# Kernel tuning notes

Measured on AMD Instinct MI355X. Metric: run time of the kernel, lower is better.

Reference implementation:

```python
import jax, jax.numpy as jnp
import numpy as np

EPS_BN = 1e-4


def gcn_conv(x, W, b, src, dst):
    """PyG GCNConv with added self-loops and symmetric normalization."""
    N = x.shape[0]
    h = x @ W  # [N, out]
    # degree over targets, +1 for the implicit self-loop on every node
    deg = jnp.zeros((N,), x.dtype).at[dst].add(1.0) + 1.0
    dinv = jax.lax.rsqrt(deg)  # deg^{-1/2}
    norm = dinv[src] * dinv[dst]  # per-edge coefficient
    msg = h[src] * norm[:, None]  # [E, out] gather (memory-bound)
    out = jax.ops.segment_sum(msg, dst, num_segments=N)
    out = out + h * (dinv * dinv)[:, None]  # self-loop term, norm = 1/deg
    return out + b


def batch_norm(x, gamma, beta):
    # training-mode BN over the node dim, biased variance (matches torch train)
    m = jnp.mean(x, axis=0)
    v = jnp.mean(jnp.square(x - m), axis=0)
    return (x - m) * jax.lax.rsqrt(v + EPS_BN) * gamma + beta


def setup_inputs() -> dict:
    key = jax.random.key(0)
    ks = jax.random.split(key, 8)
    N, E, D = 100000, 1600000, 64
    L = 2
    x = jax.random.normal(ks[0], (N, D), jnp.float32)
    edge_index = jax.random.randint(ks[1], (2, E), 0, N, jnp.int32)
    batch = jnp.sort(jax.random.randint(ks[2], (N,), 0, 128, jnp.int32))
    s = 1.0 / np.sqrt(D)
    return {
        "x": x,
        "edge_index": edge_index,
        "batch": batch,
        "enc_W": jax.random.normal(ks[3], (L, D, D), jnp.float32) * s,
        "enc_b": jnp.zeros((L, D), jnp.float32),
        "enc_gamma": jnp.ones((L, D), jnp.float32),
        "enc_beta": jnp.zeros((L, D), jnp.float32),
        "attr_W": jax.random.normal(ks[4], (L, D, D), jnp.float32) * s,
        "attr_b": jnp.zeros((L, D), jnp.float32),
        "attr_gamma": jnp.ones((L, D), jnp.float32),
        "attr_beta": jnp.zeros((L, D), jnp.float32),
        "str_W": jax.random.normal(ks[5], (L, D, D), jnp.float32) * s,
        "str_b": jnp.zeros((L, D), jnp.float32),
        "str_gamma": jnp.ones((L, D), jnp.float32),
        "str_beta": jnp.zeros((L, D), jnp.float32),
    }


def reference(x, edge_index, batch, enc_W, enc_b, enc_gamma, enc_beta,
              attr_W, attr_b, attr_gamma, attr_beta,
              str_W, str_b, str_gamma, str_beta):
    src, dst = edge_index[0], edge_index[1]
    L = enc_W.shape[0]

    # ---- Encoder: GCN -> sigmoid -> (dropout id) -> BN ----
    h = x
    for i in range(L):
        h = gcn_conv(h, enc_W[i], enc_b[i], src, dst)
        h = jax.nn.sigmoid(h)
        h = batch_norm(h, enc_gamma[i], enc_beta[i])
    x_enc = h
    # x_pool = global_mean_pool(x_enc, batch) is computed but discarded upstream

    # ---- Attribute decoder: GCN -> (dropout) -> sigmoid (except last) -> BN ----
    h = x_enc
    for i in range(L):
        h = gcn_conv(h, attr_W[i], attr_b[i], src, dst)
        if i != L - 1:
            h = jax.nn.sigmoid(h)
        h = batch_norm(h, attr_gamma[i], attr_beta[i])
    x_att = h

    # ---- Structure decoder ----
    h = x_enc
    for i in range(L):
        h = gcn_conv(h, str_W[i], str_b[i], src, dst)
        if i != L - 1:
            h = jax.nn.sigmoid(h)
        else:
            h = jax.nn.sigmoid(h * 0.5)
        h = batch_norm(h, str_gamma[i], str_beta[i])
    x_str = h

    return (x_str, x_att, x_enc)
```

## Files before the change

kernel.cpp:

```cpp
#include <hip/hip_runtime.h>

#define D 64
#define BCH 4096

typedef __attribute__((ext_vector_type(8))) _Float16 f16x8;
typedef __attribute__((ext_vector_type(4))) float f32x4;

__device__ __forceinline__ float sigmoidf_(float x) {
    return 1.0f / (1.0f + __expf(-x));
}
__device__ __forceinline__ float h2f(ushort u) {
    _Float16 h;
    __builtin_memcpy(&h, &u, 2);
    return (float)h;
}
__device__ __forceinline__ ushort f2h(float f) {
    _Float16 h = (_Float16)f;
    ushort u;
    __builtin_memcpy(&u, &h, 2);
    return u;
}
__device__ __forceinline__ float2 up2(uint v) {
    float2 r;
    r.x = h2f((ushort)(v & 0xffffu));
    r.y = h2f((ushort)(v >> 16));
    return r;
}


__global__ __launch_bounds__(256) void bin_edges(const int* __restrict__ src,
                                                 const int* __restrict__ dst,
                                                 int* __restrict__ bcur,
                                                 int* __restrict__ binsrc,
                                                 int* __restrict__ bindst,
                                                 int CAP, int E) {
    __shared__ int lsrc[BCH], ldst[BCH];
    __shared__ int hist[128], base[128];
    int t = threadIdx.x;
    int e0 = blockIdx.x * BCH;
    if (t < 128) hist[t] = 0;
    __syncthreads();
    for (int k = t; k < BCH; k += 256) {
        int e = e0 + k;
        int d_ = -1, s_ = 0;
        if (e < E) {
            s_ = src[e];
            d_ = dst[e];
            atomicAdd(&hist[d_ >> 10], 1);
        }
        lsrc[k] = s_;
        ldst[k] = d_;
    }
    __syncthreads();
    if (t < 128) {
        int c = hist[t];
        base[t] = (c > 0) ? atomicAdd(&bcur[t], c) : 0;
        hist[t] = 0;
    }
    __syncthreads();
    for (int k = t; k < BCH; k += 256) {
        int d_ = ldst[k];
        if (d_ >= 0) {
            int b = d_ >> 10;
            int p = base[b] + atomicAdd(&hist[b], 1);
            binsrc[(size_t)b * CAP + p] = lsrc[k];
            bindst[(size_t)b * CAP + p] = d_;
        }
    }
}

__global__ __launch_bounds__(128) void scan_nb(const int* __restrict__ bcur,
                                               int* __restrict__ boff,
                                               int* __restrict__ csr,
                                               int NB, int N, int E) {
    __shared__ int tmp[128];
    int t = threadIdx.x;
    int v = (t < NB) ? bcur[t] : 0;
    tmp[t] = v;
    __syncthreads();
    for (int o = 1; o < 128; o <<= 1) {
        int x = (t >= o) ? tmp[t - o] : 0;
        __syncthreads();
        tmp[t] += x;
        __syncthreads();
    }
    if (t < NB) boff[t] = tmp[t] - v;
    if (t == 0) csr[N] = E;
}

__global__ __launch_bounds__(256) void build_csr(const int* __restrict__ binsrc,
                                                 const int* __restrict__ bindst,
                                                 const int* __restrict__ bcur,
                                                 const int* __restrict__ boff,
                                                 int* __restrict__ csr,
                                                 int* __restrict__ sorted,
                                                 float* __restrict__ dinv,
                                                 float* __restrict__ rdinv,
                                                 int CAP, int N) {
    __shared__ int hist[1024];
    __shared__ int part[256];
    int t = threadIdx.x;
    int b = blockIdx.x;
    int nb0 = b << 10;
    int cnt = bcur[b];
    int e0 = boff[b];
    const int* bs = binsrc + (size_t)b * CAP;
    const int* bd = bindst + (size_t)b * CAP;
    for (int k = t; k < 1024; k += 256) hist[k] = 0;
    __syncthreads();
    for (int k = t; k < cnt; k += 256) atomicAdd(&hist[bd[k] - nb0], 1);
    __syncthreads();
    int v0 = hist[4 * t], v1 = hist[4 * t + 1], v2 = hist[4 * t + 2], v3 = hist[4 * t + 3];
    part[t] = v0 + v1 + v2 + v3;
    __syncthreads();
    for (int o = 1; o < 256; o <<= 1) {
        int x = (t >= o) ? part[t - o] : 0;
        __syncthreads();
        part[t] += x;
        __syncthreads();
    }
    int run = (t > 0) ? part[t - 1] : 0;
    int pre[4];
    pre[0] = run;
    pre[1] = run + v0;
    pre[2] = run + v0 + v1;
    pre[3] = run + v0 + v1 + v2;
    int deg[4] = {v0, v1, v2, v3};
    __syncthreads();
    hist[4 * t + 0] = e0 + pre[0];
    hist[4 * t + 1] = e0 + pre[1];
    hist[4 * t + 2] = e0 + pre[2];
    hist[4 * t + 3] = e0 + pre[3];
#pragma unroll
    for (int j = 0; j < 4; j++) {
        int node = nb0 + 4 * t + j;
        if (node < N) {
            csr[node] = e0 + pre[j];
            float c = (float)deg[j] + 1.0f;
            dinv[node] = rsqrtf(c);
            rdinv[node] = sqrtf(c);
        }
    }
    __syncthreads();
    for (int k = t; k < cnt; k += 256) {
        int d_ = bd[k];
        int p = atomicAdd(&hist[d_ - nb0], 1);
        sorted[p] = bs[k];
    }
}


__global__ __launch_bounds__(256) void prep_xd(const float* __restrict__ x,
                                               const float* __restrict__ dinv,
                                               ushort* __restrict__ actd, int N16) {
    int p = blockIdx.x * 256 + threadIdx.x;
    if (p >= N16) return;
    int n = p >> 4;
    float d = dinv[n];
    float4 v = reinterpret_cast<const float4*>(x)[p];
    ushort4 o;
    o.x = f2h(v.x * d);
    o.y = f2h(v.y * d);
    o.z = f2h(v.z * d);
    o.w = f2h(v.w * d);
    reinterpret_cast<ushort4*>(actd)[p] = o;
}

__global__ __launch_bounds__(256) void wprep(const float* __restrict__ W,
                                             ushort* __restrict__ wfrag) {
    int idx = blockIdx.x * 256 + threadIdx.x;
    if (idx >= 4096) return;
    int i = idx & 7;
    int lane = (idx >> 3) & 63;
    int hc = idx >> 9;
    int h = hc >> 2, c = hc & 3;
    int k = h * 32 + (lane >> 4) * 8 + i;
    int j = c * 16 + (lane & 15);
    wfrag[idx] = f2h(W[k * 64 + j]);
}

__global__ __launch_bounds__(256) void layer_prep(const float* __restrict__ ssum,
                                                  const float* __restrict__ sssq,
                                                  const float* __restrict__ gamma,
                                                  const float* __restrict__ beta,
                                                  const float* __restrict__ W,
                                                  float* __restrict__ A,
                                                  float* __restrict__ C,
                                                  float* __restrict__ u,
                                                  ushort* __restrict__ wfrag,
                                                  float invN) {
    __shared__ float As[64], Cs[64];
    int t = threadIdx.x;
    if (t < 64) {
        float m = ssum[t] * invN;
        float var = sssq[t] * invN - m * m;
        float rs = rsqrtf(var + 1e-4f);
        float a = rs * gamma[t];
        As[t] = a;
        A[t] = a;
        float c = fmaf(-m, a, beta[t]);
        Cs[t] = c;
        C[t] = c;
    }
    __syncthreads();
    if (t < 64) {
        float s = 0.f;
        for (int k = 0; k < 64; k++) s = fmaf(Cs[k], W[k * 64 + t], s);
        u[t] = s;
    }
    for (int idx = t; idx < 4096; idx += 256) {
        int i = idx & 7;
        int lane = (idx >> 3) & 63;
        int hc = idx >> 9;
        int h = hc >> 2, c = hc & 3;
        int k = h * 32 + (lane >> 4) * 8 + i;
        int j = c * 16 + (lane & 15);
        wfrag[idx] = f2h(W[k * 64 + j] * As[k]);
    }
}

__global__ __launch_bounds__(64) void finalize_aff(const float* __restrict__ ssum,
                                                   const float* __restrict__ sssq,
                                                   const float* __restrict__ gamma,
                                                   const float* __restrict__ beta,
                                                   float* __restrict__ A,
                                                   float* __restrict__ C, float invN) {
    int c = threadIdx.x;
    float m = ssum[c] * invN;
    float var = sssq[c] * invN - m * m;
    float rs = rsqrtf(var + 1e-4f);
    float a = rs * gamma[c];
    A[c] = a;
    C[c] = fmaf(-m, a, beta[c]);
}


__global__ __launch_bounds__(256) void agg_g(const ushort* __restrict__ actd,
                                             const int* __restrict__ ptr,
                                             const int* __restrict__ srcs,
                                             const float* __restrict__ dinv,
                                             const float* __restrict__ rdinv,
                                             ushort* __restrict__ zh,
                                             float* __restrict__ ssum,
                                             float* __restrict__ sssq,
                                             float* __restrict__ qout, int N, int E) {
    __shared__ float red[2][4][64];
    int lane = threadIdx.x & 63;
    int wv = threadIdx.x >> 6;
    int Em1 = E - 1;
    const bool do_stats = (ssum != nullptr);
    const bool do_q = (qout != nullptr);
    float ps = 0.f, pq = 0.f;
    for (int n = blockIdx.x * 4 + wv; n < N; n += gridDim.x * 4) {
        int s = ptr[n], e = ptr[n + 1];
        float self = h2f(actd[((size_t)n << 6) + lane]);
        float acc = self;
        float dn = dinv[n];
        if (do_stats) {
            float a = self * rdinv[n];
            ps += a;
            pq += a * a;
        }
        float qa = 0.f;
        int i = s;
        int idx8 = srcs[min(i + (lane & 7), Em1)];
        while (i + 8 <= e) {
            int ni = i + 8;
            int nidx = srcs[min(ni + (lane & 7), Em1)];
#pragma unroll
            for (int j = 0; j < 8; j++) {
                int u = __builtin_amdgcn_readlane(idx8, j);
                float f = h2f(actd[((size_t)u << 6) + lane]);
                acc += f;
                if (do_q) qa += dinv[u];
            }
            idx8 = nidx;
            i = ni;
        }
        if (i < e) {
#pragma unroll
            for (int j = 0; j < 8; j++) {
                int u = __builtin_amdgcn_readlane(idx8, j);
                float f = h2f(actd[((size_t)u << 6) + lane]);
                float w = (i + j < e) ? 1.0f : 0.0f;
                acc = fmaf(w, f, acc);
                if (do_q) qa = fmaf(w, dinv[u], qa);
            }
        }
        if (do_q && lane == 0) qout[n] = dn * (dn + qa);
        zh[((size_t)n << 6) + lane] = f2h(acc * dn);
    }
    if (do_stats) {
        red[0][wv][lane] = ps;
        red[1][wv][lane] = pq;
        __syncthreads();
        if (wv == 0) {
            float t0 = red[0][0][lane] + red[0][1][lane] + red[0][2][lane] + red[0][3][lane];
            float t1 = red[1][0][lane] + red[1][1][lane] + red[1][2][lane] + red[1][3][lane];
            atomicAdd(&ssum[lane], t0);
            atomicAdd(&sssq[lane], t1);
        }
    }
}

__global__ __launch_bounds__(256) void agg_dual(const ushort* __restrict__ ab,
                                                const int* __restrict__ ptr,
                                                const int* __restrict__ srcs,
                                                const float* __restrict__ dinv,
                                                const float* __restrict__ rdinv,
                                                ushort* __restrict__ zab,
                                                float* __restrict__ ssA,
                                                float* __restrict__ sqA,
                                                float* __restrict__ ssS,
                                                float* __restrict__ sqS,
                                                int N, int E) {
    __shared__ float red[2][4][128];
    int lane = threadIdx.x & 63;
    int wv = threadIdx.x >> 6;
    int Em1 = E - 1;
    float2 ps = make_float2(0.f, 0.f), pq = make_float2(0.f, 0.f);
    for (int n = blockIdx.x * 4 + wv; n < N; n += gridDim.x * 4) {
        int s = ptr[n], e = ptr[n + 1];
        uint su = *reinterpret_cast<const uint*>(ab + ((size_t)n << 7) + (lane << 1));
        float2 acc = up2(su);
        {
            float r = rdinv[n];
            float ax = acc.x * r, ay = acc.y * r;
            ps.x += ax; ps.y += ay;
            pq.x += ax * ax; pq.y += ay * ay;
        }
        int i = s;
        int idx8 = srcs[min(i + (lane & 7), Em1)];
        while (i + 8 <= e) {
            int ni = i + 8;
            int nidx = srcs[min(ni + (lane & 7), Em1)];
#pragma unroll
            for (int j = 0; j < 8; j++) {
                int u = __builtin_amdgcn_readlane(idx8, j);
                uint v = *reinterpret_cast<const uint*>(ab + ((size_t)u << 7) + (lane << 1));
                float2 f = up2(v);
                acc.x += f.x;
                acc.y += f.y;
            }
            idx8 = nidx;
            i = ni;
        }
        if (i < e) {
#pragma unroll
            for (int j = 0; j < 8; j++) {
                int u = __builtin_amdgcn_readlane(idx8, j);
                uint v = *reinterpret_cast<const uint*>(ab + ((size_t)u << 7) + (lane << 1));
                float w = (i + j < e) ? 1.0f : 0.0f;
                float2 f = up2(v);
                acc.x = fmaf(w, f.x, acc.x);
                acc.y = fmaf(w, f.y, acc.y);
            }
        }
        float dn = dinv[n];
        uint pk = (uint)f2h(acc.x * dn) | ((uint)f2h(acc.y * dn) << 16);
        *reinterpret_cast<uint*>(zab + ((size_t)n << 7) + (lane << 1)) = pk;
    }
    red[0][wv][2 * lane + 0] = ps.x;
    red[0][wv][2 * lane + 1] = ps.y;
    red[1][wv][2 * lane + 0] = pq.x;
    red[1][wv][2 * lane + 1] = pq.y;
    __syncthreads();
    if (wv == 0) {
#pragma unroll
        for (int m0 = 0; m0 < 2; m0++) {
            int m = lane + m0 * 64;
            float t0 = red[0][0][m] + red[0][1][m] + red[0][2][m] + red[0][3][m];
            float t1 = red[1][0][m] + red[1][1][m] + red[1][2][m] + red[1][3][m];
            if (m < 64) {
                atomicAdd(&ssA[m], t0);
                atomicAdd(&sqA[m], t1);
            } else {
                atomicAdd(&ssS[m - 64], t0);
                atomicAdd(&sqS[m - 64], t1);
            }
        }
    }
}

template <int MODE, bool HAS_AFF, int OM>
__global__ __launch_bounds__(256) void gemm_mfma(const ushort* __restrict__ zh, int is,
                                                 const ushort* __restrict__ wfrag,
                                                 const float* __restrict__ bias,
                                                 const float* __restrict__ u,
                                                 const float* __restrict__ q,
                                                 const float* __restrict__ dinv,
                                                 ushort* __restrict__ outh, int os,
                                                 float* __restrict__ outf,
                                                 float* __restrict__ s0,
                                                 float* __restrict__ s1, int N) {
    int tid = threadIdx.x;
    int lane = tid & 63;
    int wv = tid >> 6;
    int l15 = lane & 15;
    int lg = lane >> 4;
    int tb = blockIdx.x * 64;

    const ushort* zrow = zh + (size_t)(tb + wv * 16 + l15) * is + (lg << 3);
    f16x8 a0 = *reinterpret_cast<const f16x8*>(zrow);
    f16x8 a1 = *reinterpret_cast<const f16x8*>(zrow + 32);

    const f16x8* wf = reinterpret_cast<const f16x8*>(wfrag) + lane;

    f32x4 acc[4];
#pragma unroll
    for (int c = 0; c < 4; c++) {
        f32x4 t = {0.f, 0.f, 0.f, 0.f};
        t = __builtin_amdgcn_mfma_f32_16x16x32_f16(a0, wf[(0 * 4 + c) * 64], t, 0, 0, 0);
        t = __builtin_amdgcn_mfma_f32_16x16x32_f16(a1, wf[(1 * 4 + c) * 64], t, 0, 0, 0);
        acc[c] = t;
    }

    int rowbase = tb + wv * 16 + lg * 4;
    float qv[4], dv[4];
    bool vld[4];
#pragma unroll
    for (int r = 0; r < 4; r++) {
        int row = rowbase + r;
        vld[r] = row < N;
        qv[r] = (HAS_AFF && vld[r]) ? q[row] : 0.f;
        dv[r] = (OM == 0 && vld[r]) ? dinv[row] : 0.f;
    }
    float sa[4], sq[4];
#pragma unroll
    for (int c = 0; c < 4; c++) { sa[c] = 0.f; sq[c] = 0.f; }

#pragma unroll
    for (int c = 0; c < 4; c++) {
        int col = c * 16 + l15;
        float bcol = bias[col];
        float ucol = HAS_AFF ? u[col] : 0.f;
        float Acol = (OM == 2) ? s0[col] : 0.f;
        float Ccol = (OM == 2) ? s1[col] : 0.f;
#pragma unroll
        for (int r = 0; r < 4; r++) {
            if (!vld[r]) continue;
            float o = acc[c][r] + bcol;
            if (HAS_AFF) o = fmaf(qv[r], ucol, o);
            float a = (MODE == 0) ? sigmoidf_(o)
// ... 66 lines not shown
    for (int c = 0; c < 4; c++) {
        f32x4 t = {0.f, 0.f, 0.f, 0.f};
        t = __builtin_amdgcn_mfma_f32_16x16x32_f16(a0, wa[(0 * 4 + c) * 64], t, 0, 0, 0);
        t = __builtin_amdgcn_mfma_f32_16x16x32_f16(a1, wa[(1 * 4 + c) * 64], t, 0, 0, 0);
        accA[c] = t;
        f32x4 t2 = {0.f, 0.f, 0.f, 0.f};
        t2 = __builtin_amdgcn_mfma_f32_16x16x32_f16(a0, wsp[(0 * 4 + c) * 64], t2, 0, 0, 0);
        t2 = __builtin_amdgcn_mfma_f32_16x16x32_f16(a1, wsp[(1 * 4 + c) * 64], t2, 0, 0, 0);
        accS[c] = t2;
    }

    int rowbase = tb + wv * 16 + lg * 4;
    float qv[4], dv[4];
    bool vld[4];
#pragma unroll
    for (int r = 0; r < 4; r++) {
        int row = rowbase + r;
        vld[r] = row < N;
        qv[r] = vld[r] ? q[row] : 0.f;
        dv[r] = vld[r] ? dinv[row] : 0.f;
    }
#pragma unroll
    for (int c = 0; c < 4; c++) {
        int col = c * 16 + l15;
        float bcA = bA[col], ucA = uA[col];
        float bcS = bS[col], ucS = uS[col];
#pragma unroll
        for (int r = 0; r < 4; r++) {
            if (!vld[r]) continue;
            int row = rowbase + r;
            float oA = fmaf(qv[r], ucA, accA[c][r] + bcA);
            float oS = fmaf(qv[r], ucS, accS[c][r] + bcS);
            float aA = sigmoidf_(oA);
            float aS = sigmoidf_(oS);
            outAB[((size_t)row << 7) + col] = f2h(aA * dv[r]);
            outAB[((size_t)row << 7) + 64 + col] = f2h(aS * dv[r]);
        }
    }
}

__global__ __launch_bounds__(256) void bn_apply_h(const ushort* __restrict__ actd,
                                                  const float* __restrict__ rdinv,
                                                  const float* __restrict__ A,
                                                  const float* __restrict__ C,
                                                  float* __restrict__ out, int N16) {
    int p = blockIdx.x * 256 + threadIdx.x;
    if (p >= N16) return;
    int n = p >> 4;
    int cb = (p & 15) * 4;
    float r = rdinv[n];
    ushort4 v = reinterpret_cast<const ushort4*>(actd)[p];
    float4 o;
    o.x = fmaf(h2f(v.x) * r, A[cb + 0], C[cb + 0]);
    o.y = fmaf(h2f(v.y) * r, A[cb + 1], C[cb + 1]);
    o.z = fmaf(h2f(v.z) * r, A[cb + 2], C[cb + 2]);
    o.w = fmaf(h2f(v.w) * r, A[cb + 3], C[cb + 3]);
    reinterpret_cast<float4*>(out)[p] = o;
}


extern "C" void kernel_launch(void* const* d_in, const int* in_sizes, int n_in,
                              void* d_out, int out_size, void* d_ws, size_t ws_size,
                              hipStream_t stream) {
    const int N = in_sizes[0] / D;
    const int E = in_sizes[1] / 2;

    const float* x = (const float*)d_in[0];
    const int* ei = (const int*)d_in[1];
    const int* src_in = ei;
    const int* dst_in = ei + E;
    const float* encW = (const float*)d_in[3];
    const float* encb = (const float*)d_in[4];
    const float* encg = (const float*)d_in[5];
    const float* encbe = (const float*)d_in[6];
    const float* attW = (const float*)d_in[7];
    const float* attb = (const float*)d_in[8];
    const float* attg = (const float*)d_in[9];
    const float* attbe = (const float*)d_in[10];
    const float* strW = (const float*)d_in[11];
    const float* strb = (const float*)d_in[12];
    const float* strg = (const float*)d_in[13];
    const float* strbe = (const float*)d_in[14];

    const int NB = (N + 1023) >> 10;
    int CAP = (E + NB - 1) / NB;
    CAP = CAP + CAP / 8 + 256;
    CAP = (CAP + 255) & ~255;

    char* ws = (char*)d_ws;
    size_t off = 0;
    auto alloc = [&](size_t bytes) -> char* {
        char* p = ws + off;
        off += (bytes + 255) & ~(size_t)255;
        return p;
    };
    int* csr = (int*)alloc((size_t)(N + 1) * 4);
    int* bcur = (int*)alloc(128 * 4);
    int* boff = (int*)alloc(128 * 4);
    float* dinv = (float*)alloc((size_t)N * 4);
    float* rdinv = (float*)alloc((size_t)N * 4);
    float* q = (float*)alloc((size_t)N * 4);
    float* stats = (float*)alloc(6 * 128 * 4);
    float* aff = (float*)alloc(6 * 128 * 4);
    float* ubuf = (float*)alloc(6 * 64 * 4);
    ushort* wf = (ushort*)alloc(6 * 4096 * 2);
    int* sorted = (int*)alloc((size_t)E * 4);
    ushort* zh = (ushort*)alloc((size_t)(N + 64) * 64 * 2);
    size_t binbytes = 2 * (size_t)NB * CAP * 4;
    size_t zabbytes = (size_t)(N + 64) * 128 * 2;
    char* region = alloc(binbytes > zabbytes ? binbytes : zabbytes);
    int* binsrc = (int*)region;
    int* bindst = binsrc + (size_t)NB * CAP;
    ushort* zab = (ushort*)region;
    ushort* hA = (ushort*)alloc((size_t)N * 64 * 2);
    ushort* hB = (ushort*)alloc((size_t)N * 64 * 2);
    ushort* hAB = (ushort*)alloc((size_t)(N + 64) * 128 * 2);

    float* out_str = (float*)d_out;
    float* out_att = out_str + (size_t)N * D;
    float* out_enc = out_att + (size_t)N * D;

    hipMemsetAsync(bcur, 0, 128 * 4, stream);
    hipMemsetAsync(stats, 0, 6 * 128 * 4, stream);

    int N16 = N * 16;
    int g16 = (N16 + 255) / 256;
    int gT = (N + 63) / 64;
    float invN = 1.0f / (float)N;

    float* A0 = aff + 0 * 128; float* C0 = A0 + 64;
    float* A1 = aff + 1 * 128; float* C1 = A1 + 64;
    float* A2 = aff + 2 * 128; float* C2 = A2 + 64;
    float* A3 = aff + 3 * 128; float* C3 = A3 + 64;
    float* A4 = aff + 4 * 128; float* C4 = A4 + 64;
    float* A5 = aff + 5 * 128; float* C5 = A5 + 64;
    ushort* wf0 = wf + 0 * 4096;
    ushort* wf1 = wf + 1 * 4096;
    ushort* wf2 = wf + 2 * 4096;
    ushort* wf3 = wf + 3 * 4096;
    ushort* wf4 = wf + 4 * 4096;
    ushort* wf5 = wf + 5 * 4096;

    bin_edges<<<(E + BCH - 1) / BCH, 256, 0, stream>>>(src_in, dst_in, bcur,
                                                       binsrc, bindst, CAP, E);
    scan_nb<<<1, 128, 0, stream>>>(bcur, boff, csr, NB, N, E);
    build_csr<<<NB, 256, 0, stream>>>(binsrc, bindst, bcur, boff, csr, sorted,
                                      dinv, rdinv, CAP, N);

    prep_xd<<<g16, 256, 0, stream>>>(x, dinv, hA, N16);
    wprep<<<16, 256, 0, stream>>>(encW, wf0);
    agg_g<<<2048, 256, 0, stream>>>(hA, csr, sorted, dinv, rdinv, zh,
                                    nullptr, nullptr, q, N, E);
    gemm_mfma<0, false, 0><<<gT, 256, 0, stream>>>(zh, 64, wf0, encb, nullptr,
                                                   q, dinv, hB, 64, nullptr,
                                                   nullptr, nullptr, N);
    agg_g<<<2048, 256, 0, stream>>>(hB, csr, sorted, dinv, rdinv, zh,
                                    stats + 0, stats + 64, nullptr, N, E);
    layer_prep<<<1, 256, 0, stream>>>(stats + 0, stats + 64, encg, encbe,
                                      encW + 4096, A0, C0, ubuf + 0, wf1, invN);
    gemm_mfma<0, true, 0><<<gT, 256, 0, stream>>>(zh, 64, wf1, encb + 64, ubuf + 0,
                                                  q, dinv, hA, 64, nullptr,
                                                  nullptr, nullptr, N);
    agg_g<<<2048, 256, 0, stream>>>(hA, csr, sorted, dinv, rdinv, zh,
                                    stats + 128, stats + 192, nullptr, N, E);
    layer_prep<<<1, 256, 0, stream>>>(stats + 128, stats + 192, encg + 64,
                                      encbe + 64, attW, A1, C1, ubuf + 64, wf2, invN);
    layer_prep<<<1, 256, 0, stream>>>(stats + 128, stats + 192, encg + 64,
                                      encbe + 64, strW, A1, C1, ubuf + 128, wf3, invN);
    bn_apply_h<<<g16, 256, 0, stream>>>(hA, rdinv, A1, C1, out_enc, N16);
    gemm_dual<<<gT, 256, 0, stream>>>(zh, wf2, wf3, attb, strb, ubuf + 64,
                                      ubuf + 128, q, dinv, hAB, N);
    agg_dual<<<2048, 256, 0, stream>>>(hAB, csr, sorted, dinv, rdinv, zab,
                                       stats + 256, stats + 320,
                                       stats + 512, stats + 576, N, E);
    layer_prep<<<1, 256, 0, stream>>>(stats + 256, stats + 320, attg, attbe,
                                      attW + 4096, A2, C2, ubuf + 192, wf4, invN);
    gemm_mfma<1, true, 1><<<gT, 256, 0, stream>>>(zab, 128, wf4, attb + 64,
                                                  ubuf + 192, q, dinv, nullptr, 0,
                                                  nullptr, stats + 384, stats + 448, N);
    finalize_aff<<<1, 64, 0, stream>>>(stats + 384, stats + 448, attg + 64,
                                       attbe + 64, A3, C3, invN);
    gemm_mfma<1, true, 2><<<gT, 256, 0, stream>>>(zab, 128, wf4, attb + 64,
                                                  ubuf + 192, q, dinv, nullptr, 0,
                                                  out_att, A3, C3, N);
    layer_prep<<<1, 256, 0, stream>>>(stats + 512, stats + 576, strg, strbe,
                                      strW + 4096, A4, C4, ubuf + 320, wf5, invN);
    gemm_mfma<2, true, 1><<<gT, 256, 0, stream>>>(zab + 64, 128, wf5, strb + 64,
                                                  ubuf + 320, q, dinv, nullptr, 0,
                                                  nullptr, stats + 640, stats + 704, N);
    finalize_aff<<<1, 64, 0, stream>>>(stats + 640, stats + 704, strg + 64,
                                       strbe + 64, A5, C5, invN);
    gemm_mfma<2, true, 2><<<gT, 256, 0, stream>>>(zab + 64, 128, wf5, strb + 64,
                                                  ubuf + 320, q, dinv, nullptr, 0,
                                                  out_str, A5, C5, N);
}
```

Baseline: 604.9 us.

## Pack edge bins into single word and interleave two nodes per wave in aggregation

Edge binning now packs the source index and the low 10 bits of the destination into one 32-bit word, which halves the global traffic for binned edges and the local memory used by the binning kernel. Both aggregation kernels now have each wave process two nodes from opposite halves of the node range in an interleaved loop. This puts more independent gathers in flight per wave to hide memory latency. The cost is more registers and divergent control flow when the two nodes' degrees differ, and the packing assumes the source index fits in 22 bits.

```diff
diff --git a/kernel.cpp b/kernel.cpp
--- a/kernel.cpp
+++ b/kernel.cpp
@@ -31,10 +31,10 @@
 __global__ __launch_bounds__(256) void bin_edges(const int* __restrict__ src,
                                                  const int* __restrict__ dst,
                                                  int* __restrict__ bcur,
-                                                 int* __restrict__ binsrc,
-                                                 int* __restrict__ bindst,
+                                                 uint* __restrict__ bins,
                                                  int CAP, int E) {
-    __shared__ int lsrc[BCH], ldst[BCH];
+    __shared__ uint lp[BCH];
+    __shared__ unsigned char lb[BCH];
     __shared__ int hist[128], base[128];
     int t = threadIdx.x;
     int e0 = blockIdx.x * BCH;
@@ -42,14 +42,17 @@
     __syncthreads();
     for (int k = t; k < BCH; k += 256) {
         int e = e0 + k;
-        int d_ = -1, s_ = 0;
+        uint p = 0xFFFFFFFFu;
+        int b = 0;
         if (e < E) {
-            s_ = src[e];
-            d_ = dst[e];
-            atomicAdd(&hist[d_ >> 10], 1);
-        }
-        lsrc[k] = s_;
-        ldst[k] = d_;
+            int s_ = src[e];
+            int d_ = dst[e];
+            b = d_ >> 10;
+            atomicAdd(&hist[b], 1);
+            p = ((uint)s_ << 10) | (uint)(d_ & 1023);
+        }
+        lp[k] = p;
+        lb[k] = (unsigned char)b;
     }
     __syncthreads();
     if (t < 128) {
@@ -59,12 +62,11 @@
     }
     __syncthreads();
     for (int k = t; k < BCH; k += 256) {
-        int d_ = ldst[k];
-        if (d_ >= 0) {
-            int b = d_ >> 10;
-            int p = base[b] + atomicAdd(&hist[b], 1);
-            binsrc[(size_t)b * CAP + p] = lsrc[k];
-            bindst[(size_t)b * CAP + p] = d_;
+        uint p = lp[k];
+        if (p != 0xFFFFFFFFu) {
+            int b = lb[k];
+            int pos = base[b] + atomicAdd(&hist[b], 1);
+            bins[(size_t)b * CAP + pos] = p;
         }
     }
 }
@@ -88,8 +90,7 @@
     if (t == 0) csr[N] = E;
 }
 
-__global__ __launch_bounds__(256) void build_csr(const int* __restrict__ binsrc,
-                                                 const int* __restrict__ bindst,
+__global__ __launch_bounds__(256) void build_csr(const uint* __restrict__ bins,
                                                  const int* __restrict__ bcur,
                                                  const int* __restrict__ boff,
                                                  int* __restrict__ csr,
@@ -104,11 +105,10 @@
     int nb0 = b << 10;
     int cnt = bcur[b];
     int e0 = boff[b];
-    const int* bs = binsrc + (size_t)b * CAP;
-    const int* bd = bindst + (size_t)b * CAP;
+    const uint* bp = bins + (size_t)b * CAP;
     for (int k = t; k < 1024; k += 256) hist[k] = 0;
     __syncthreads();
-    for (int k = t; k < cnt; k += 256) atomicAdd(&hist[bd[k] - nb0], 1);
+    for (int k = t; k < cnt; k += 256) atomicAdd(&hist[bp[k] & 1023u], 1);
     __syncthreads();
     int v0 = hist[4 * t], v1 = hist[4 * t + 1], v2 = hist[4 * t + 2], v3 = hist[4 * t + 3];
     part[t] = v0 + v1 + v2 + v3;
@@ -143,9 +143,9 @@
     }
     __syncthreads();
     for (int k = t; k < cnt; k += 256) {
-        int d_ = bd[k];
-        int p = atomicAdd(&hist[d_ - nb0], 1);
-        sorted[p] = bs[k];
+        uint p = bp[k];
+        int pos = atomicAdd(&hist[p & 1023u], 1);
+        sorted[pos] = (int)(p >> 10);
     }
 }
 
@@ -247,48 +247,106 @@
     __shared__ float red[2][4][64];
     int lane = threadIdx.x & 63;
     int wv = threadIdx.x >> 6;
+    int l7 = lane & 7;
     int Em1 = E - 1;
     const bool do_stats = (ssum != nullptr);
     const bool do_q = (qout != nullptr);
     float ps = 0.f, pq = 0.f;
-    for (int n = blockIdx.x * 4 + wv; n < N; n += gridDim.x * 4) {
-        int s = ptr[n], e = ptr[n + 1];
-        float self = h2f(actd[((size_t)n << 6) + lane]);
-        float acc = self;
-        float dn = dinv[n];
+    int Nh = (N + 1) >> 1;
+    for (int n0 = blockIdx.x * 4 + wv; n0 < Nh; n0 += gridDim.x * 4) {
+        int nA = n0;
+        int nB = n0 + Nh;
+        bool hasB = nB < N;
+        int sA = ptr[nA], eA = ptr[nA + 1];
+        int sB = 0, eB = 0;
+        if (hasB) { sB = ptr[nB]; eB = ptr[nB + 1]; }
+        float selfA = h2f(actd[((size_t)nA << 6) + lane]);
+        float accA = selfA;
+        float dnA = dinv[nA];
+        float accB = 0.f, dnB = 0.f;
+        if (hasB) {
+            float selfB = h2f(actd[((size_t)nB << 6) + lane]);
+            accB = selfB;
+            dnB = dinv[nB];
+            if (do_stats) {
+                float rb = rdinv[nB];
+                float b = selfB * rb;
+                ps += b;
+                pq += b * b;
+            }
+        }
         if (do_stats) {
-            float a = self * rdinv[n];
+            float ra = rdinv[nA];
+            float a = selfA * ra;
             ps += a;
             pq += a * a;
         }
-        float qa = 0.f;
-        int i = s;
-        int idx8 = srcs[min(i + (lane & 7), Em1)];
-        while (i + 8 <= e) {
-            int ni = i + 8;
-            int nidx = srcs[min(ni + (lane & 7), Em1)];
+        float qaA = 0.f, qaB = 0.f;
+        int iA = sA, iB = sB;
+        int idxA = srcs[min(iA + l7, Em1)];
+        int idxB = hasB ? srcs[min(iB + l7, Em1)] : 0;
+        while (iA + 8 <= eA || iB + 8 <= eB) {
+            bool gA = iA + 8 <= eA;
+            bool gB = iB + 8 <= eB;
+            ushort ua[8], ub[8];
+            if (gA) {
+#pragma unroll
+                for (int j = 0; j < 8; j++) {
+                    int u = __builtin_amdgcn_readlane(idxA, j);
+                    ua[j] = actd[((size_t)u << 6) + lane];
+                    if (do_q) qaA += dinv[u];
+                }
+            }
+            if (gB) {
+#pragma unroll
+                for (int j = 0; j < 8; j++) {
+                    int u = __builtin_amdgcn_readlane(idxB, j);
+                    ub[j] = actd[((size_t)u << 6) + lane];
+                    if (do_q) qaB += dinv[u];
+                }
+            }
+            int idxA2 = idxA, idxB2 = idxB;
+            if (gA) idxA2 = srcs[min(iA + 8 + l7, Em1)];
+            if (gB) idxB2 = srcs[min(iB + 8 + l7, Em1)];
+            if (gA) {
+                accA += ((h2f(ua[0]) + h2f(ua[1])) + (h2f(ua[2]) + h2f(ua[3]))) +
+                        ((h2f(ua[4]) + h2f(ua[5])) + (h2f(ua[6]) + h2f(ua[7])));
+                iA += 8;
+                idxA = idxA2;
+            }
+            if (gB) {
+                accB += ((h2f(ub[0]) + h2f(ub[1])) + (h2f(ub[2]) + h2f(ub[3]))) +
+                        ((h2f(ub[4]) + h2f(ub[5])) + (h2f(ub[6]) + h2f(ub[7])));
+                iB += 8;
+                idxB = idxB2;
+            }
+        }
+        if (iA < eA) {
 #pragma unroll
             for (int j = 0; j < 8; j++) {
-                int u = __builtin_amdgcn_readlane(idx8, j);
+                int u = __builtin_amdgcn_readlane(idxA, j);
+                float w = (iA + j < eA) ? 1.0f : 0.0f;
                 float f = h2f(actd[((size_t)u << 6) + lane]);
-                acc += f;
-                if (do_q) qa += dinv[u];
-            }
-            idx8 = nidx;
-            i = ni;
-        }
-        if (i < e) {
+                accA = fmaf(w, f, accA);
+                if (do_q) qaA = fmaf(w, dinv[u], qaA);
+            }
+        }
+        if (hasB && iB < eB) {
 #pragma unroll
             for (int j = 0; j < 8; j++) {
-                int u = __builtin_amdgcn_readlane(idx8, j);
+                int u = __builtin_amdgcn_readlane(idxB, j);
+                float w = (iB + j < eB) ? 1.0f : 0.0f;
                 float f = h2f(actd[((size_t)u << 6) + lane]);
-                float w = (i + j < e) ? 1.0f : 0.0f;
-                acc = fmaf(w, f, acc);
-                if (do_q) qa = fmaf(w, dinv[u], qa);
-            }
-        }
-        if (do_q && lane == 0) qout[n] = dn * (dn + qa);
-        zh[((size_t)n << 6) + lane] = f2h(acc * dn);
+                accB = fmaf(w, f, accB);
+                if (do_q) qaB = fmaf(w, dinv[u], qaB);
+            }
+        }
+        if (do_q && lane == 0) {
+            qout[nA] = dnA * (dnA + qaA);
+            if (hasB) qout[nB] = dnB * (dnB + qaB);
+        }
+        zh[((size_t)nA << 6) + lane] = f2h(accA * dnA);
+        if (hasB) zh[((size_t)nB << 6) + lane] = f2h(accB * dnB);
     }
     if (do_stats) {
         red[0][wv][lane] = ps;
@@ -317,48 +375,110 @@
     __shared__ float red[2][4][128];
     int lane = threadIdx.x & 63;
     int wv = threadIdx.x >> 6;
+    int l7 = lane & 7;
     int Em1 = E - 1;
     float2 ps = make_float2(0.f, 0.f), pq = make_float2(0.f, 0.f);
-    for (int n = blockIdx.x * 4 + wv; n < N; n += gridDim.x * 4) {
-        int s = ptr[n], e = ptr[n + 1];
-        uint su = *reinterpret_cast<const uint*>(ab + ((size_t)n << 7) + (lane << 1));
-        float2 acc = up2(su);
+    int Nh = (N + 1) >> 1;
+    for (int n0 = blockIdx.x * 4 + wv; n0 < Nh; n0 += gridDim.x * 4) {
+        int nA = n0;
+        int nB = n0 + Nh;
+        bool hasB = nB < N;
+        int sA = ptr[nA], eA = ptr[nA + 1];
+        int sB = 0, eB = 0;
+        if (hasB) { sB = ptr[nB]; eB = ptr[nB + 1]; }
+        uint suA = *reinterpret_cast<const uint*>(ab + ((size_t)nA << 7) + (lane << 1));
+        float2 accA = up2(suA);
+        float dnA = dinv[nA];
         {
-            float r = rdinv[n];
-            float ax = acc.x * r, ay = acc.y * r;
+            float r = rdinv[nA];
+            float ax = accA.x * r, ay = accA.y * r;
             ps.x += ax; ps.y += ay;
             pq.x += ax * ax; pq.y += ay * ay;
         }
-        int i = s;
-        int idx8 = srcs[min(i + (lane & 7), Em1)];
-        while (i + 8 <= e) {
-            int ni = i + 8;
-            int nidx = srcs[min(ni + (lane & 7), Em1)];
+        float2 accB = make_float2(0.f, 0.f);
+        float dnB = 0.f;
+        if (hasB) {
+            uint suB = *reinterpret_cast<const uint*>(ab + ((size_t)nB << 7) + (lane << 1));
+            accB = up2(suB);
+            dnB = dinv[nB];
+            float r = rdinv[nB];
+            float ax = accB.x * r, ay = accB.y * r;
+            ps.x += ax; ps.y += ay;
+            pq.x += ax * ax; pq.y += ay * ay;
+        }
+        int iA = sA, iB = sB;
+        int idxA = srcs[min(iA + l7, Em1)];
+        int idxB = hasB ? srcs[min(iB + l7, Em1)] : 0;
+        while (iA + 8 <= eA || iB + 8 <= eB) {
+            bool gA = iA + 8 <= eA;
+            bool gB = iB + 8 <= eB;
+            uint va[8], vb[8];
+            if (gA) {
+#pragma unroll
+                for (int j = 0; j < 8; j++) {
+                    int u = __builtin_amdgcn_readlane(idxA, j);
+                    va[j] = *reinterpret_cast<const uint*>(ab + ((size_t)u << 7) + (lane << 1));
+                }
+            }
+            if (gB) {
+#pragma unroll
+                for (int j = 0; j < 8; j++) {
+                    int u = __builtin_amdgcn_readlane(idxB, j);
+                    vb[j] = *reinterpret_cast<const uint*>(ab + ((size_t)u << 7) + (lane << 1));
+                }
+            }
+            int idxA2 = idxA, idxB2 = idxB;
+            if (gA) idxA2 = srcs[min(iA + 8 + l7, Em1)];
+            if (gB) idxB2 = srcs[min(iB + 8 + l7, Em1)];
+            if (gA) {
+#pragma unroll
+                for (int j = 0; j < 8; j++) {
+                    float2 f = up2(va[j]);
+                    accA.x += f.x;
+                    accA.y += f.y;
+                }
+                iA += 8;
+                idxA = idxA2;
+            }
+            if (gB) {
+#pragma unroll
+                for (int j = 0; j < 8; j++) {
+                    float2 f = up2(vb[j]);
+                    accB.x += f.x;
+                    accB.y += f.y;
+                }
+                iB += 8;
+                idxB = idxB2;
+            }
+        }
+        if (iA < eA) {
 #pragma unroll
             for (int j = 0; j < 8; j++) {
-                int u = __builtin_amdgcn_readlane(idx8, j);
+                int u = __builtin_amdgcn_readlane(idxA, j);
                 uint v = *reinterpret_cast<const uint*>(ab + ((size_t)u << 7) + (lane << 1));
+                float w = (iA + j < eA) ? 1.0f : 0.0f;
                 float2 f = up2(v);
-                acc.x += f.x;
-                acc.y += f.y;
-            }
-            idx8 = nidx;
-            i = ni;
-        }
-        if (i < e) {
+                accA.x = fmaf(w, f.x, accA.x);
+                accA.y = fmaf(w, f.y, accA.y);
+            }
+        }
+        if (hasB && iB < eB) {
 #pragma unroll
             for (int j = 0; j < 8; j++) {
-                int u = __builtin_amdgcn_readlane(idx8, j);
+                int u = __builtin_amdgcn_readlane(idxB, j);
                 uint v = *reinterpret_cast<const uint*>(ab + ((size_t)u << 7) + (lane << 1));
-                float w = (i + j < e) ? 1.0f : 0.0f;
+                float w = (iB + j < eB) ? 1.0f : 0.0f;
                 float2 f = up2(v);
-                acc.x = fmaf(w, f.x, acc.x);
-                acc.y = fmaf(w, f.y, acc.y);
-            }
-        }
-        float dn = dinv[n];
-        uint pk = (uint)f2h(acc.x * dn) | ((uint)f2h(acc.y * dn) << 16);
-        *reinterpret_cast<uint*>(zab + ((size_t)n << 7) + (lane << 1)) = pk;
+                accB.x = fmaf(w, f.x, accB.x);
+                accB.y = fmaf(w, f.y, accB.y);
+            }
+        }
+        uint pkA = (uint)f2h(accA.x * dnA) | ((uint)f2h(accA.y * dnA) << 16);
+        *reinterpret_cast<uint*>(zab + ((size_t)nA << 7) + (lane << 1)) = pkA;
+        if (hasB) {
+            uint pkB = (uint)f2h(accB.x * dnB) | ((uint)f2h(accB.y * dnB) << 16);
+            *reinterpret_cast<uint*>(zab + ((size_t)nB << 7) + (lane << 1)) = pkB;
+        }
     }
     red[0][wv][2 * lane + 0] = ps.x;
     red[0][wv][2 * lane + 1] = ps.y;
@@ -615,11 +735,10 @@
     ushort* wf = (ushort*)alloc(6 * 4096 * 2);
     int* sorted = (int*)alloc((size_t)E * 4);
     ushort* zh = (ushort*)alloc((size_t)(N + 64) * 64 * 2);
-    size_t binbytes = 2 * (size_t)NB * CAP * 4;
+    size_t binbytes = (size_t)NB * CAP * 4;
     size_t zabbytes = (size_t)(N + 64) * 128 * 2;
     char* region = alloc(binbytes > zabbytes ? binbytes : zabbytes);
-    int* binsrc = (int*)region;
-    int* bindst = binsrc + (size_t)NB * CAP;
+    uint* bins = (uint*)region;
     ushort* zab = (ushort*)region;
     ushort* hA = (ushort*)alloc((size_t)N * 64 * 2);
     ushort* hB = (ushort*)alloc((size_t)N * 64 * 2);
@@ -651,9 +770,9 @@
     ushort* wf5 = wf + 5 * 4096;
 
     bin_edges<<<(E + BCH - 1) / BCH, 256, 0, stream>>>(src_in, dst_in, bcur,
-                                                       binsrc, bindst, CAP, E);
+                                                       bins, CAP, E);
     scan_nb<<<1, 128, 0, stream>>>(bcur, boff, csr, NB, N, E);
-    build_csr<<<NB, 256, 0, stream>>>(binsrc, bindst, bcur, boff, csr, sorted,
+    build_csr<<<NB, 256, 0, stream>>>(bins, bcur, boff, csr, sorted,
                                       dinv, rdinv, CAP, N);
 
     prep_xd<<<g16, 256, 0, stream>>>(x, dinv, hA, N16);
```

After: 602.8 us. About the same (-0.3%).

## Partition CSR edges by source slab to improve gather locality

Applied to the files above, without the earlier changes.

Edges are now binned by (source slab of 8192 nodes, destination block), producing 16 separate CSR segments per node so that the edges stored in each bin come from a narrow source range. Aggregation kernels walk the 16 segments in order, aiming to keep gathered feature rows within a cache-friendly window. Bins pack src and local dst into one 32-bit word, and degree/dinv moves to a separate kernel summing the 16 segment lengths. This costs 16 CSR pointer reads per node, many short segments with partial 8-edge groups, and a loss of cross-group index prefetch in the gather loop.

```diff
diff --git a/kernel.cpp b/kernel.cpp
--- a/kernel.cpp
+++ b/kernel.cpp
@@ -2,6 +2,8 @@
 
 #define D 64
 #define BCH 4096
+#define NS 16
+#define SSH 13
 
 typedef __attribute__((ext_vector_type(8))) _Float16 f16x8;
 typedef __attribute__((ext_vector_type(4))) float f32x4;
@@ -31,84 +33,102 @@
 __global__ __launch_bounds__(256) void bin_edges(const int* __restrict__ src,
                                                  const int* __restrict__ dst,
                                                  int* __restrict__ bcur,
-                                                 int* __restrict__ binsrc,
-                                                 int* __restrict__ bindst,
-                                                 int CAP, int E) {
-    __shared__ int lsrc[BCH], ldst[BCH];
-    __shared__ int hist[128], base[128];
+                                                 uint* __restrict__ bins,
+                                                 int CAP, int NBd, int NB2, int E) {
+    __shared__ uint lp[BCH];
+    __shared__ ushort lb[BCH];
+    __shared__ int hist[1600], base[1600];
     int t = threadIdx.x;
     int e0 = blockIdx.x * BCH;
-    if (t < 128) hist[t] = 0;
+    for (int k = t; k < NB2; k += 256) hist[k] = 0;
     __syncthreads();
     for (int k = t; k < BCH; k += 256) {
         int e = e0 + k;
-        int d_ = -1, s_ = 0;
+        uint p = 0xFFFFFFFFu;
+        int b = 0;
         if (e < E) {
-            s_ = src[e];
-            d_ = dst[e];
-            atomicAdd(&hist[d_ >> 10], 1);
-        }
-        lsrc[k] = s_;
-        ldst[k] = d_;
-    }
-    __syncthreads();
-    if (t < 128) {
-        int c = hist[t];
-        base[t] = (c > 0) ? atomicAdd(&bcur[t], c) : 0;
-        hist[t] = 0;
+            int s_ = src[e];
+            int d_ = dst[e];
+            b = (s_ >> SSH) * NBd + (d_ >> 10);
+            atomicAdd(&hist[b], 1);
+            p = ((uint)s_ << 10) | (uint)(d_ & 1023);
+        }
+        lp[k] = p;
+        lb[k] = (ushort)b;
+    }
+    __syncthreads();
+    for (int k = t; k < NB2; k += 256) {
+        int c = hist[k];
+        base[k] = (c > 0) ? atomicAdd(&bcur[k], c) : 0;
+        hist[k] = 0;
     }
     __syncthreads();
     for (int k = t; k < BCH; k += 256) {
-        int d_ = ldst[k];
-        if (d_ >= 0) {
-            int b = d_ >> 10;
-            int p = base[b] + atomicAdd(&hist[b], 1);
-            binsrc[(size_t)b * CAP + p] = lsrc[k];
-            bindst[(size_t)b * CAP + p] = d_;
-        }
-    }
-}
-
-__global__ __launch_bounds__(128) void scan_nb(const int* __restrict__ bcur,
-                                               int* __restrict__ boff,
-                                               int* __restrict__ csr,
-                                               int NB, int N, int E) {
-    __shared__ int tmp[128];
+        uint p = lp[k];
+        if (p != 0xFFFFFFFFu) {
+            int b = lb[k];
+            int pos = base[b] + atomicAdd(&hist[b], 1);
+            bins[(size_t)b * CAP + pos] = p;
+        }
+    }
+}
+
+__global__ __launch_bounds__(256) void scan2(const int* __restrict__ bcur,
+                                             int* __restrict__ boff,
+                                             int* __restrict__ csr4,
+                                             int NBd, int NB2, int N, int E) {
+    __shared__ int part[256];
     int t = threadIdx.x;
-    int v = (t < NB) ? bcur[t] : 0;
-    tmp[t] = v;
-    __syncthreads();
-    for (int o = 1; o < 128; o <<= 1) {
-        int x = (t >= o) ? tmp[t - o] : 0;
+    int sum8 = 0;
+#pragma unroll
+    for (int i = 0; i < 8; i++) {
+        int idx = t * 8 + i;
+        if (idx < NB2) sum8 += bcur[idx];
+    }
+    part[t] = sum8;
+    __syncthreads();
+    for (int o = 1; o < 256; o <<= 1) {
+        int x = (t >= o) ? part[t - o] : 0;
         __syncthreads();
-        tmp[t] += x;
+        part[t] += x;
         __syncthreads();
     }
-    if (t < NB) boff[t] = tmp[t] - v;
-    if (t == 0) csr[N] = E;
-}
-
-__global__ __launch_bounds__(256) void build_csr(const int* __restrict__ binsrc,
-                                                 const int* __restrict__ bindst,
+    int run = part[t] - sum8;
+#pragma unroll
+    for (int i = 0; i < 8; i++) {
+        int idx = t * 8 + i;
+        if (idx < NB2) {
+            boff[idx] = run;
+            run += bcur[idx];
+        }
+    }
+    __syncthreads();
+    if (t < NS) {
+        size_t NP1 = (size_t)N + 1;
+        int endv = (t + 1 < NS) ? boff[(t + 1) * NBd] : E;
+        csr4[t * NP1 + N] = endv;
+    }
+}
+
+__global__ __launch_bounds__(256) void build_csr(const uint* __restrict__ bins,
                                                  const int* __restrict__ bcur,
                                                  const int* __restrict__ boff,
-                                                 int* __restrict__ csr,
+                                                 int* __restrict__ csr4,
                                                  int* __restrict__ sorted,
-                                                 float* __restrict__ dinv,
-                                                 float* __restrict__ rdinv,
-                                                 int CAP, int N) {
+                                                 int CAP, int NBd, int N) {
     __shared__ int hist[1024];
     __shared__ int part[256];
     int t = threadIdx.x;
     int b = blockIdx.x;
-    int nb0 = b << 10;
+    int s = b / NBd;
+    int dloc0 = (b % NBd) << 10;
+    size_t NP1 = (size_t)N + 1;
     int cnt = bcur[b];
     int e0 = boff[b];
-    const int* bs = binsrc + (size_t)b * CAP;
-    const int* bd = bindst + (size_t)b * CAP;
+    const uint* bp = bins + (size_t)b * CAP;
     for (int k = t; k < 1024; k += 256) hist[k] = 0;
     __syncthreads();
-    for (int k = t; k < cnt; k += 256) atomicAdd(&hist[bd[k] - nb0], 1);
+    for (int k = t; k < cnt; k += 256) atomicAdd(&hist[bp[k] & 1023u], 1);
     __syncthreads();
     int v0 = hist[4 * t], v1 = hist[4 * t + 1], v2 = hist[4 * t + 2], v3 = hist[4 * t + 3];
     part[t] = v0 + v1 + v2 + v3;
@@ -125,7 +145,6 @@
     pre[1] = run + v0;
     pre[2] = run + v0 + v1;
     pre[3] = run + v0 + v1 + v2;
-    int deg[4] = {v0, v1, v2, v3};
     __syncthreads();
     hist[4 * t + 0] = e0 + pre[0];
     hist[4 * t + 1] = e0 + pre[1];
@@ -133,20 +152,29 @@
     hist[4 * t + 3] = e0 + pre[3];
 #pragma unroll
     for (int j = 0; j < 4; j++) {
-        int node = nb0 + 4 * t + j;
-        if (node < N) {
-            csr[node] = e0 + pre[j];
-            float c = (float)deg[j] + 1.0f;
-            dinv[node] = rsqrtf(c);
-            rdinv[node] = sqrtf(c);
-        }
+        int node = dloc0 + 4 * t + j;
+        if (node < N) csr4[s * NP1 + node] = e0 + pre[j];
     }
     __syncthreads();
     for (int k = t; k < cnt; k += 256) {
-        int d_ = bd[k];
-        int p = atomicAdd(&hist[d_ - nb0], 1);
-        sorted[p] = bs[k];
-    }
+        uint p = bp[k];
+        int pos = atomicAdd(&hist[p & 1023u], 1);
+        sorted[pos] = (int)(p >> 10);
+    }
+}
+
+__global__ __launch_bounds__(256) void deg_dinv(const int* __restrict__ csr4,
+                                                float* __restrict__ dinv,
+                                                float* __restrict__ rdinv, int N) {
+    int n = blockIdx.x * 256 + threadIdx.x;
+    if (n >= N) return;
+    size_t NP1 = (size_t)N + 1;
+    int deg = 0;
+    for (int s = 0; s < NS; s++)
+        deg += csr4[s * NP1 + n + 1] - csr4[s * NP1 + n];
+    float c = (float)deg + 1.0f;
+    dinv[n] = rsqrtf(c);
+    rdinv[n] = sqrtf(c);
 }
 
 
@@ -236,7 +264,7 @@
 
 
 __global__ __launch_bounds__(256) void agg_g(const ushort* __restrict__ actd,
-                                             const int* __restrict__ ptr,
+                                             const int* __restrict__ csr4,
                                              const int* __restrict__ srcs,
                                              const float* __restrict__ dinv,
                                              const float* __restrict__ rdinv,
@@ -247,12 +275,13 @@
     __shared__ float red[2][4][64];
     int lane = threadIdx.x & 63;
     int wv = threadIdx.x >> 6;
+    int l7 = lane & 7;
     int Em1 = E - 1;
     const bool do_stats = (ssum != nullptr);
     const bool do_q = (qout != nullptr);
+    size_t NP1 = (size_t)N + 1;
     float ps = 0.f, pq = 0.f;
     for (int n = blockIdx.x * 4 + wv; n < N; n += gridDim.x * 4) {
-        int s = ptr[n], e = ptr[n + 1];
         float self = h2f(actd[((size_t)n << 6) + lane]);
         float acc = self;
         float dn = dinv[n];
@@ -262,29 +291,42 @@
             pq += a * a;
         }
         float qa = 0.f;
-        int i = s;
-        int idx8 = srcs[min(i + (lane & 7), Em1)];
-        while (i + 8 <= e) {
-            int ni = i + 8;
-            int nidx = srcs[min(ni + (lane & 7), Em1)];
-#pragma unroll
-            for (int j = 0; j < 8; j++) {
-                int u = __builtin_amdgcn_readlane(idx8, j);
-                float f = h2f(actd[((size_t)u << 6) + lane]);
-                acc += f;
-                if (do_q) qa += dinv[u];
-            }
-            idx8 = nidx;
-            i = ni;
-        }
-        if (i < e) {
-#pragma unroll
-            for (int j = 0; j < 8; j++) {
-                int u = __builtin_amdgcn_readlane(idx8, j);
-                float f = h2f(actd[((size_t)u << 6) + lane]);
-                float w = (i + j < e) ? 1.0f : 0.0f;
-                acc = fmaf(w, f, acc);
-                if (do_q) qa = fmaf(w, dinv[u], qa);
+        for (int s = 0; s < NS; s++) {
+            int sb = csr4[s * NP1 + n];
+            int d = csr4[s * NP1 + n + 1] - sb;
+            while (d > 0) {
+                int take = (d > 8) ? 8 : d;
+                int idx8 = srcs[min(sb + l7, Em1)];
+                if (take == 8) {
+                    float t0, t1, t2, t3, t4, t5, t6, t7;
+                    int u0 = __builtin_amdgcn_readlane(idx8, 0);
+                    int u1 = __builtin_amdgcn_readlane(idx8, 1);
+                    int u2 = __builtin_amdgcn_readlane(idx8, 2);
+                    int u3 = __builtin_amdgcn_readlane(idx8, 3);
+                    int u4 = __builtin_amdgcn_readlane(idx8, 4);
+                    int u5 = __builtin_amdgcn_readlane(idx8, 5);
+                    int u6 = __builtin_amdgcn_readlane(idx8, 6);
+                    int u7 = __builtin_amdgcn_readlane(idx8, 7);
+                    t0 = h2f(actd[((size_t)u0 << 6) + lane]);
+                    t1 = h2f(actd[((size_t)u1 << 6) + lane]);
+                    t2 = h2f(actd[((size_t)u2 << 6) + lane]);
+                    t3 = h2f(actd[((size_t)u3 << 6) + lane]);
+                    t4 = h2f(actd[((size_t)u4 << 6) + lane]);
+                    t5 = h2f(actd[((size_t)u5 << 6) + lane]);
+                    t6 = h2f(actd[((size_t)u6 << 6) + lane]);
+                    t7 = h2f(actd[((size_t)u7 << 6) + lane]);
+                    if (do_q) qa += ((dinv[u0] + dinv[u1]) + (dinv[u2] + dinv[u3])) +
+                                    ((dinv[u4] + dinv[u5]) + (dinv[u6] + dinv[u7]));
+                    acc += ((t0 + t1) + (t2 + t3)) + ((t4 + t5) + (t6 + t7));
+                } else {
+                    for (int j = 0; j < take; j++) {
+                        int u = __builtin_amdgcn_readlane(idx8, j);
+                        acc += h2f(actd[((size_t)u << 6) + lane]);
+                        if (do_q) qa += dinv[u];
+                    }
+                }
+                sb += take;
+                d -= take;
             }
         }
         if (do_q && lane == 0) qout[n] = dn * (dn + qa);
@@ -304,7 +346,7 @@
 }
 
 __global__ __launch_bounds__(256) void agg_dual(const ushort* __restrict__ ab,
-                                                const int* __restrict__ ptr,
+                                                const int* __restrict__ csr4,
                                                 const int* __restrict__ srcs,
                                                 const float* __restrict__ dinv,
                                                 const float* __restrict__ rdinv,
@@ -317,46 +359,61 @@
     __shared__ float red[2][4][128];
     int lane = threadIdx.x & 63;
     int wv = threadIdx.x >> 6;
+    int l7 = lane & 7;
     int Em1 = E - 1;
+    size_t NP1 = (size_t)N + 1;
     float2 ps = make_float2(0.f, 0.f), pq = make_float2(0.f, 0.f);
     for (int n = blockIdx.x * 4 + wv; n < N; n += gridDim.x * 4) {
-        int s = ptr[n], e = ptr[n + 1];
         uint su = *reinterpret_cast<const uint*>(ab + ((size_t)n << 7) + (lane << 1));
         float2 acc = up2(su);
+        float dn = dinv[n];
         {
             float r = rdinv[n];
             float ax = acc.x * r, ay = acc.y * r;
             ps.x += ax; ps.y += ay;
             pq.x += ax * ax; pq.y += ay * ay;
         }
-        int i = s;
-        int idx8 = srcs[min(i + (lane & 7), Em1)];
-        while (i + 8 <= e) {
-            int ni = i + 8;
-            int nidx = srcs[min(ni + (lane & 7), Em1)];
-#pragma unroll
-            for (int j = 0; j < 8; j++) {
-                int u = __builtin_amdgcn_readlane(idx8, j);
-                uint v = *reinterpret_cast<const uint*>(ab + ((size_t)u << 7) + (lane << 1));
-                float2 f = up2(v);
-                acc.x += f.x;
-                acc.y += f.y;
+        for (int s = 0; s < NS; s++) {
+            int sb = csr4[s * NP1 + n];
+            int d = csr4[s * NP1 + n + 1] - sb;
+            while (d > 0) {
+                int take = (d > 8) ? 8 : d;
+                int idx8 = srcs[min(sb + l7, Em1)];
+                if (take == 8) {
+                    uint v0, v1, v2, v3, v4, v5, v6, v7;
+                    int u0 = __builtin_amdgcn_readlane(idx8, 0);
+                    int u1 = __builtin_amdgcn_readlane(idx8, 1);
+                    int u2 = __builtin_amdgcn_readlane(idx8, 2);
+                    int u3 = __builtin_amdgcn_readlane(idx8, 3);
+                    int u4 = __builtin_amdgcn_readlane(idx8, 4);
+                    int u5 = __builtin_amdgcn_readlane(idx8, 5);
+                    int u6 = __builtin_amdgcn_readlane(idx8, 6);
+                    int u7 = __builtin_amdgcn_readlane(idx8, 7);
+                    v0 = *reinterpret_cast<const uint*>(ab + ((size_t)u0 << 7) + (lane << 1));
+                    v1 = *reinterpret_cast<const uint*>(ab + ((size_t)u1 << 7) + (lane << 1));
+                    v2 = *reinterpret_cast<const uint*>(ab + ((size_t)u2 << 7) + (lane << 1));
+                    v3 = *reinterpret_cast<const uint*>(ab + ((size_t)u3 << 7) + (lane << 1));
+                    v4 = *reinterpret_cast<const uint*>(ab + ((size_t)u4 << 7) + (lane << 1));
+                    v5 = *reinterpret_cast<const uint*>(ab + ((size_t)u5 << 7) + (lane << 1));
+                    v6 = *reinterpret_cast<const uint*>(ab + ((size_t)u6 << 7) + (lane << 1));
+                    v7 = *reinterpret_cast<const uint*>(ab + ((size_t)u7 << 7) + (lane << 1));
+                    float2 f0 = up2(v0), f1 = up2(v1), f2 = up2(v2), f3 = up2(v3);
+                    float2 f4 = up2(v4), f5 = up2(v5), f6 = up2(v6), f7 = up2(v7);
+                    acc.x += ((f0.x + f1.x) + (f2.x + f3.x)) + ((f4.x + f5.x) + (f6.x + f7.x));
+                    acc.y += ((f0.y + f1.y) + (f2.y + f3.y)) + ((f4.y + f5.y) + (f6.y + f7.y));
+                } else {
+                    for (int j = 0; j < take; j++) {
+                        int u = __builtin_amdgcn_readlane(idx8, j);
+                        uint v = *reinterpret_cast<const uint*>(ab + ((size_t)u << 7) + (lane << 1));
+                        float2 f = up2(v);
+                        acc.x += f.x;
+                        acc.y += f.y;
+                    }
+                }
+                sb += take;
+                d -= take;
             }
-            idx8 = nidx;
-            i = ni;
-        }
-        if (i < e) {
-#pragma unroll
-            for (int j = 0; j < 8; j++) {
-                int u = __builtin_amdgcn_readlane(idx8, j);
-                uint v = *reinterpret_cast<const uint*>(ab + ((size_t)u << 7) + (lane << 1));
-                float w = (i + j < e) ? 1.0f : 0.0f;
-                float2 f = up2(v);
-                acc.x = fmaf(w, f.x, acc.x);
-                acc.y = fmaf(w, f.y, acc.y);
-            }
-        }
-        float dn = dinv[n];
+        }
         uint pk = (uint)f2h(acc.x * dn) | ((uint)f2h(acc.y * dn) << 16);
         *reinterpret_cast<uint*>(zab + ((size_t)n << 7) + (lane << 1)) = pk;
     }
@@ -591,9 +648,10 @@
     const float* strg = (const float*)d_in[13];
     const float* strbe = (const float*)d_in[14];
 
-    const int NB = (N + 1023) >> 10;
-    int CAP = (E + NB - 1) / NB;
-    CAP = CAP + CAP / 8 + 256;
+    const int NBd = (N + 1023) >> 10;
+    const int NB2 = NS * NBd;
+    int CAP = (E + NB2 - 1) / NB2;
+    CAP = CAP + CAP / 4 + 128;
     CAP = (CAP + 255) & ~255;
 
     char* ws = (char*)d_ws;
@@ -603,9 +661,9 @@
         off += (bytes + 255) & ~(size_t)255;
         return p;
     };
-    int* csr = (int*)alloc((size_t)(N + 1) * 4);
-    int* bcur = (int*)alloc(128 * 4);
-    int* boff = (int*)alloc(128 * 4);
+    int* csr4 = (int*)alloc((size_t)NS * (N + 1) * 4);
+    int* bcur = (int*)alloc(2048 * 4);
+    int* boff = (int*)alloc(2048 * 4);
     float* dinv = (float*)alloc((size_t)N * 4);
     float* rdinv = (float*)alloc((size_t)N * 4);
     float* q = (float*)alloc((size_t)N * 4);
@@ -615,11 +673,10 @@
     ushort* wf = (ushort*)alloc(6 * 4096 * 2);
     int* sorted = (int*)alloc((size_t)E * 4);
     ushort* zh = (ushort*)alloc((size_t)(N + 64) * 64 * 2);
-    size_t binbytes = 2 * (size_t)NB * CAP * 4;
+    size_t binbytes = (size_t)NB2 * CAP * 4;
     size_t zabbytes = (size_t)(N + 64) * 128 * 2;
     char* region = alloc(binbytes > zabbytes ? binbytes : zabbytes);
-    int* binsrc = (int*)region;
-    int* bindst = binsrc + (size_t)NB * CAP;
+    uint* bins = (uint*)region;
     ushort* zab = (ushort*)region;
     ushort* hA = (ushort*)alloc((size_t)N * 64 * 2);
     ushort* hB = (ushort*)alloc((size_t)N * 64 * 2);
@@ -629,11 +686,12 @@
     float* out_att = out_str + (size_t)N * D;
     float* out_enc = out_att + (size_t)N * D;
 
-    hipMemsetAsync(bcur, 0, 128 * 4, stream);
+    hipMemsetAsync(bcur, 0, 2048 * 4, stream);
     hipMemsetAsync(stats, 0, 6 * 128 * 4, stream);
 
     int N16 = N * 16;
     int g16 = (N16 + 255) / 256;
+    int gN = (N + 255) / 256;
     int gT = (N + 63) / 64;
     float invN = 1.0f / (float)N;
 
@@ -651,26 +709,27 @@
     ushort* wf5 = wf + 5 * 4096;
 
     bin_edges<<<(E + BCH - 1) / BCH, 256, 0, stream>>>(src_in, dst_in, bcur,
-                                                       binsrc, bindst, CAP, E);
-    scan_nb<<<1, 128, 0, stream>>>(bcur, boff, csr, NB, N, E);
-    build_csr<<<NB, 256, 0, stream>>>(binsrc, bindst, bcur, boff, csr, sorted,
-                                      dinv, rdinv, CAP, N);
+                                                       bins, CAP, NBd, NB2, E);
+    scan2<<<1, 256, 0, stream>>>(bcur, boff, csr4, NBd, NB2, N, E);
+    build_csr<<<NB2, 256, 0, stream>>>(bins, bcur, boff, csr4, sorted,
+                                       CAP, NBd, N);
+    deg_dinv<<<gN, 256, 0, stream>>>(csr4, dinv, rdinv, N);
 
     prep_xd<<<g16, 256, 0, stream>>>(x, dinv, hA, N16);
     wprep<<<16, 256, 0, stream>>>(encW, wf0);
-    agg_g<<<2048, 256, 0, stream>>>(hA, csr, sorted, dinv, rdinv, zh,
+    agg_g<<<2048, 256, 0, stream>>>(hA, csr4, sorted, dinv, rdinv, zh,
                                     nullptr, nullptr, q, N, E);
     gemm_mfma<0, false, 0><<<gT, 256, 0, stream>>>(zh, 64, wf0, encb, nullptr,
                                                    q, dinv, hB, 64, nullptr,
                                                    nullptr, nullptr, N);
-    agg_g<<<2048, 256, 0, stream>>>(hB, csr, sorted, dinv, rdinv, zh,
+    agg_g<<<2048, 256, 0, stream>>>(hB, csr4, sorted, dinv, rdinv, zh,
                                     stats + 0, stats + 64, nullptr, N, E);
     layer_prep<<<1, 256, 0, stream>>>(stats + 0, stats + 64, encg, encbe,
                                       encW + 4096, A0, C0, ubuf + 0, wf1, invN);
     gemm_mfma<0, true, 0><<<gT, 256, 0, stream>>>(zh, 64, wf1, encb + 64, ubuf + 0,
                                                   q, dinv, hA, 64, nullptr,
                                                   nullptr, nullptr, N);
-    agg_g<<<2048, 256, 0, stream>>>(hA, csr, sorted, dinv, rdinv, zh,
+    agg_g<<<2048, 256, 0, stream>>>(hA, csr4, sorted, dinv, rdinv, zh,
                                     stats + 128, stats + 192, nullptr, N, E);
     layer_prep<<<1, 256, 0, stream>>>(stats + 128, stats + 192, encg + 64,
                                       encbe + 64, attW, A1, C1, ubuf + 64, wf2, invN);
@@ -679,7 +738,7 @@
     bn_apply_h<<<g16, 256, 0, stream>>>(hA, rdinv, A1, C1, out_enc, N16);
     gemm_dual<<<gT, 256, 0, stream>>>(zh, wf2, wf3, attb, strb, ubuf + 64,
                                       ubuf + 128, q, dinv, hAB, N);
-    agg_dual<<<2048, 256, 0, stream>>>(hAB, csr, sorted, dinv, rdinv, zab,
+    agg_dual<<<2048, 256, 0, stream>>>(hAB, csr4, sorted, dinv, rdinv, zab,
                                        stats + 256, stats + 320,
                                        stats + 512, stats + 576, N, E);
     layer_prep<<<1, 256, 0, stream>>>(stats + 256, stats + 320, attg, attbe,
```

Measured after the change: 1.078 ms. +78.3%, slower.
